# Optimization experiments

Hardware: AMD Instinct MI355X
Metric: run time of the kernel (lower is better)

## Reference

```python
import jax, jax.numpy as jnp
import numpy as np
from jax import lax

B, S, DIMS, T, K = 4, 4096, 2048, 10, 2


def setup_inputs() -> dict:
    key = jax.random.key(0)
    ks = jax.random.split(key, 4)
    scale = 1.0 / np.sqrt(DIMS)
    x = jax.random.normal(ks[0], (B, S, DIMS), dtype=jnp.float32)
    W_cls = jax.random.normal(ks[1], (DIMS, T), dtype=jnp.float32) * scale
    W_sparse = jax.random.normal(ks[2], (DIMS, T), dtype=jnp.float32) * scale
    W_gates = jax.random.normal(ks[3], (DIMS, T), dtype=jnp.float32) * scale
    return {
        "x": x,
        "W_cls": W_cls, "b_cls": jnp.zeros((T,), jnp.float32),
        "W_sparse": W_sparse, "b_sparse": jnp.zeros((T,), jnp.float32),
        "W_gates": W_gates, "b_gates": jnp.zeros((T,), jnp.float32),
        "alpha": jnp.ones((1,), jnp.float32),
    }


def reference(x, W_cls, b_cls, W_sparse, b_sparse, W_gates, b_gates, alpha):
    # soft routing: softmax classifier over num_types
    soft_types = jax.nn.softmax(jnp.einsum("bsd,dt->bst", x, W_cls) + b_cls, axis=-1)
    # sparse routing: top-k over logits, softmax over the k kept logits,
    # scattered back into a dense [B,S,T] gate vector (zeros elsewhere)
    logits = jnp.einsum("bsd,dt->bst", x, W_sparse) + b_sparse
    top_v, top_i = lax.top_k(logits, K)                      # [B,S,K]
    sparse_g = jax.nn.softmax(top_v, axis=-1)                # [B,S,K]
    # scatter via one-hot (K and T are tiny)
    sparse_types = jnp.sum(jax.nn.one_hot(top_i, T, dtype=x.dtype) * sparse_g[..., None], axis=-2)  # [B,S,T]
    # per-type sigmoid gates: batched single matmul == stack of Linear(dims,1)+Sigmoid
    gates = jax.nn.sigmoid(jnp.einsum("bsd,dt->bst", x, W_gates) + b_gates)  # [B,S,T]
    a = jax.nn.sigmoid(alpha)                                # [1], broadcasts
    mixed_types = a * sparse_types + (1.0 - a) * soft_types  # [B,S,T]
    # original: gates stacked as [B,S,1,T], mixed unsqueezed to [B,S,1,T], sum over T -> [B,S,1]
    return jnp.sum(gates * mixed_types, axis=-1, keepdims=True)
```

## Files before the change

kernel.cpp:

```cpp
#include <hip/hip_runtime.h>
#include <math.h>


#define NROWS   16384
#define DIMS_   2048
#define TT      10
#define WAVES   4
#define BLOCK   (WAVES * 64)
#define DGRP    8
#define DPW     (DIMS_ / DGRP / WAVES)
#define DC      16
#define NCH     (DPW / DC)
#define PITCH   17

__global__ __launch_bounds__(BLOCK)
void tgate_k1(const float* __restrict__ x,
              const float* __restrict__ W_cls,
              const float* __restrict__ W_sparse,
              const float* __restrict__ W_gates,
              float* __restrict__ ws)
{
    __shared__ float tile[WAVES * 64 * PITCH];

    const int tid  = threadIdx.x;
    const int lane = tid & 63;
    const int wv   = __builtin_amdgcn_readfirstlane(tid >> 6);
    const int row0 = blockIdx.x * 64;
    const int d0   = blockIdx.y * (DIMS_ / DGRP) + wv * DPW;
    float* tile_w  = &tile[wv * 64 * PITCH];

    float acc[30];
    #pragma unroll
    for (int j = 0; j < 30; ++j) acc[j] = 0.0f;

    const float4* x4 = reinterpret_cast<const float4*>(x);
    const int rl = lane >> 2;
    const int c4 = lane & 3;

    float4 pre[4];
    #pragma unroll
    for (int i = 0; i < 4; ++i) {
        int rr = i * 16 + rl;
        pre[i] = x4[(size_t)(row0 + rr) * (DIMS_ / 4) + (d0 >> 2) + c4];
    }

    for (int c = 0; c < NCH; ++c) {
        #pragma unroll
        for (int i = 0; i < 4; ++i) {
            int rr = i * 16 + rl;
            float* dst = tile_w + rr * PITCH + c4 * 4;
            dst[0] = pre[i].x; dst[1] = pre[i].y; dst[2] = pre[i].z; dst[3] = pre[i].w;
        }
        if (c + 1 < NCH) {
            #pragma unroll
            for (int i = 0; i < 4; ++i) {
                int rr = i * 16 + rl;
                pre[i] = x4[(size_t)(row0 + rr) * (DIMS_ / 4) + ((d0 + (c + 1) * DC) >> 2) + c4];
            }
        }
        const int dg = d0 + c * DC;
        #pragma unroll
        for (int dd = 0; dd < DC; ++dd) {
            float xv = tile_w[lane * PITCH + dd];
            const float* wc = W_cls    + (size_t)(dg + dd) * TT;
            const float* wsp= W_sparse + (size_t)(dg + dd) * TT;
            const float* wg = W_gates  + (size_t)(dg + dd) * TT;
            #pragma unroll
            for (int t = 0; t < TT; ++t) acc[t]      = fmaf(xv, wc[t],  acc[t]);
            #pragma unroll
            for (int t = 0; t < TT; ++t) acc[10 + t] = fmaf(xv, wsp[t], acc[10 + t]);
            #pragma unroll
            for (int t = 0; t < TT; ++t) acc[20 + t] = fmaf(xv, wg[t],  acc[20 + t]);
        }
    }

    float* part = tile;
    __syncthreads();
    if (wv >= 2) {
        float* p = part + (size_t)((wv - 2) * 64 + lane) * 31;
        #pragma unroll
        for (int j = 0; j < 30; ++j) p[j] = acc[j];
    }
    __syncthreads();
    if (wv < 2) {
        const float* p = part + (size_t)(wv * 64 + lane) * 31;
        #pragma unroll
        for (int j = 0; j < 30; ++j) acc[j] += p[j];
    }
    __syncthreads();
    if (wv == 1) {
        float* p = part + (size_t)lane * 31;
        #pragma unroll
        for (int j = 0; j < 30; ++j) p[j] = acc[j];
    }
    __syncthreads();
    if (wv == 0) {
        const float* p = part + (size_t)lane * 31;
        #pragma unroll
        for (int j = 0; j < 30; ++j) acc[j] += p[j];
        float4* w4 = reinterpret_cast<float4*>(ws);
        size_t base = ((size_t)blockIdx.y * NROWS + row0 + lane) * 8;
        #pragma unroll
        for (int q = 0; q < 8; ++q) {
            float a0 = (q * 4 + 0 < 30) ? acc[q * 4 + 0] : 0.0f;
            float a1 = (q * 4 + 1 < 30) ? acc[q * 4 + 1] : 0.0f;
            float a2 = (q * 4 + 2 < 30) ? acc[q * 4 + 2] : 0.0f;
            float a3 = (q * 4 + 3 < 30) ? acc[q * 4 + 3] : 0.0f;
            w4[base + q] = make_float4(a0, a1, a2, a3);
        }
    }
}

__global__ __launch_bounds__(256)
void tgate_k2(const float* __restrict__ ws,
              const float* __restrict__ b_cls,
              const float* __restrict__ b_sparse,
              const float* __restrict__ b_gates,
              const float* __restrict__ alpha,
              float* __restrict__ out)
{
    const int r = blockIdx.x * 256 + threadIdx.x;
    const float4* w4 = reinterpret_cast<const float4*>(ws);

    float l[32];
    #pragma unroll
    for (int j = 0; j < 32; ++j) l[j] = 0.0f;
    #pragma unroll
    for (int s = 0; s < DGRP; ++s) {
        size_t base = ((size_t)s * NROWS + r) * 8;
        #pragma unroll
        for (int q = 0; q < 8; ++q) {
            float4 v = w4[base + q];
            l[q * 4 + 0] += v.x; l[q * 4 + 1] += v.y;
            l[q * 4 + 2] += v.z; l[q * 4 + 3] += v.w;
        }
    }

    float lc[TT], lsp[TT], g[TT];
    #pragma unroll
    for (int t = 0; t < TT; ++t) {
        lc[t]  = l[t]      + b_cls[t];
        lsp[t] = l[10 + t] + b_sparse[t];
        float lg = l[20 + t] + b_gates[t];
        g[t] = 1.0f / (1.0f + __expf(-lg));
    }
    float m = lc[0];
    #pragma unroll
    for (int t = 1; t < TT; ++t) m = fmaxf(m, lc[t]);
    float esum = 0.0f, gdot = 0.0f;
    #pragma unroll
    for (int t = 0; t < TT; ++t) {
        float e = __expf(lc[t] - m);
        esum += e;
        gdot = fmaf(g[t], e, gdot);
    }
    float v1 = lsp[0], v2 = -1e30f, gv1 = g[0], gv2 = 0.0f;
    #pragma unroll
    for (int t = 1; t < TT; ++t) {
        if (lsp[t] > v1)      { v2 = v1; gv2 = gv1; v1 = lsp[t]; gv1 = g[t]; }
        else if (lsp[t] > v2) { v2 = lsp[t]; gv2 = g[t]; }
    }
    float s1 = 1.0f / (1.0f + __expf(v2 - v1));
    float s2 = 1.0f - s1;
    float a  = 1.0f / (1.0f + __expf(-alpha[0]));
    float sparse_dot = fmaf(gv1, s1, gv2 * s2);
    out[r] = fmaf(a, sparse_dot, (1.0f - a) * (gdot / esum));
}

extern "C" void kernel_launch(void* const* d_in, const int* in_sizes, int n_in,
                              void* d_out, int out_size, void* d_ws, size_t ws_size,
                              hipStream_t stream) {
    const float* x        = (const float*)d_in[0];
    const float* W_cls    = (const float*)d_in[1];
    const float* b_cls    = (const float*)d_in[2];
    const float* W_sparse = (const float*)d_in[3];
    const float* b_sparse = (const float*)d_in[4];
    const float* W_gates  = (const float*)d_in[5];
    const float* b_gates  = (const float*)d_in[6];
    const float* alpha    = (const float*)d_in[7];
    float* out = (float*)d_out;
    float* ws  = (float*)d_ws;

    dim3 g1(NROWS / 64, DGRP);
    tgate_k1<<<g1, dim3(BLOCK), 0, stream>>>(x, W_cls, W_sparse, W_gates, ws);

    dim3 g2(NROWS / 256);
    tgate_k2<<<g2, dim3(256), 0, stream>>>(ws, b_cls, b_sparse, b_gates, alpha, out);
}
```

Measured before the change: 250.8 us.

## Stage weights in LDS and register-tile four rows per lane

Each block now covers 256 rows instead of 64. It stages its slice of all three weight matrices into shared memory, packed at 32 floats per dim so they can be read as float4. Each lane accumulates four rows, so every weight read is reused across four rows instead of being reloaded per row from global or scalar memory. The x tile is stored transposed so the per-dim reads are conflict-free. The cross-wave reduction and the workspace layout (now SoA by q-slot) are rewritten to match. The change uses 120 accumulator registers per lane, which risks lower occupancy or spills, and the grid shrinks to 512 blocks.

```diff
diff --git a/kernel.cpp b/kernel.cpp
--- a/kernel.cpp
+++ b/kernel.cpp
@@ -8,10 +8,12 @@
 #define WAVES   4
 #define BLOCK   (WAVES * 64)
 #define DGRP    8
-#define DPW     (DIMS_ / DGRP / WAVES)
-#define DC      16
+#define DBLK    (DIMS_ / DGRP)
+#define DPW     (DBLK / WAVES)
+#define DC      8
 #define NCH     (DPW / DC)
-#define PITCH   17
+#define RPB     256
+#define RPL     4
 
 __global__ __launch_bounds__(BLOCK)
 void tgate_k1(const float* __restrict__ x,
@@ -20,94 +22,133 @@
               const float* __restrict__ W_gates,
               float* __restrict__ ws)
 {
-    __shared__ float tile[WAVES * 64 * PITCH];
+    __shared__ float xt[WAVES][DC][RPB];
+    __shared__ float Wl[DBLK * 32];
 
     const int tid  = threadIdx.x;
     const int lane = tid & 63;
     const int wv   = __builtin_amdgcn_readfirstlane(tid >> 6);
-    const int row0 = blockIdx.x * 64;
-    const int d0   = blockIdx.y * (DIMS_ / DGRP) + wv * DPW;
-    float* tile_w  = &tile[wv * 64 * PITCH];
-
-    float acc[30];
-    #pragma unroll
-    for (int j = 0; j < 30; ++j) acc[j] = 0.0f;
+    const int row0 = blockIdx.x * RPB;
+    const int gy   = blockIdx.y;
+    const int d0w  = gy * DBLK + wv * DPW;
+
+    {
+        const float* Wm[3] = { W_cls, W_sparse, W_gates };
+        #pragma unroll
+        for (int m = 0; m < 3; ++m) {
+            const float* src = Wm[m] + (size_t)gy * DBLK * TT;
+            #pragma unroll
+            for (int it = 0; it < DBLK * TT / BLOCK; ++it) {
+                int f = it * BLOCK + tid;
+                int d = f / TT, t = f - d * TT;
+                Wl[d * 32 + m * TT + t] = src[f];
+            }
+        }
+    }
+
+    float acc[RPL][TT * 3];
+    #pragma unroll
+    for (int r = 0; r < RPL; ++r)
+        #pragma unroll
+        for (int j = 0; j < 30; ++j) acc[r][j] = 0.0f;
 
     const float4* x4 = reinterpret_cast<const float4*>(x);
-    const int rl = lane >> 2;
-    const int c4 = lane & 3;
-
-    float4 pre[4];
-    #pragma unroll
-    for (int i = 0; i < 4; ++i) {
-        int rr = i * 16 + rl;
-        pre[i] = x4[(size_t)(row0 + rr) * (DIMS_ / 4) + (d0 >> 2) + c4];
-    }
+    const int rhalf = lane >> 1;
+    const int dpart = (lane & 1) * 4;
+
+    float4 pre[8];
+    #pragma unroll
+    for (int i = 0; i < 8; ++i)
+        pre[i] = x4[(size_t)(row0 + i * 32 + rhalf) * (DIMS_ / 4) + ((d0w + dpart) >> 2)];
+
+    __syncthreads();
 
     for (int c = 0; c < NCH; ++c) {
         #pragma unroll
-        for (int i = 0; i < 4; ++i) {
-            int rr = i * 16 + rl;
-            float* dst = tile_w + rr * PITCH + c4 * 4;
-            dst[0] = pre[i].x; dst[1] = pre[i].y; dst[2] = pre[i].z; dst[3] = pre[i].w;
+        for (int i = 0; i < 8; ++i) {
+            int rl = i * 32 + rhalf;
+            xt[wv][dpart + 0][rl] = pre[i].x;
+            xt[wv][dpart + 1][rl] = pre[i].y;
+            xt[wv][dpart + 2][rl] = pre[i].z;
+            xt[wv][dpart + 3][rl] = pre[i].w;
         }
         if (c + 1 < NCH) {
             #pragma unroll
-            for (int i = 0; i < 4; ++i) {
-                int rr = i * 16 + rl;
-                pre[i] = x4[(size_t)(row0 + rr) * (DIMS_ / 4) + ((d0 + (c + 1) * DC) >> 2) + c4];
+            for (int i = 0; i < 8; ++i)
+                pre[i] = x4[(size_t)(row0 + i * 32 + rhalf) * (DIMS_ / 4)
+                            + ((d0w + (c + 1) * DC + dpart) >> 2)];
+        }
+        const int dl0 = wv * DPW + c * DC;
+        #pragma unroll
+        for (int dd = 0; dd < DC; ++dd) {
+            float xv[RPL];
+            #pragma unroll
+            for (int r = 0; r < RPL; ++r) xv[r] = xt[wv][dd][lane + 64 * r];
+            const float4* wr = reinterpret_cast<const float4*>(&Wl[(dl0 + dd) * 32]);
+            #pragma unroll
+            for (int q = 0; q < 8; ++q) {
+                float4 w = wr[q];
+                #pragma unroll
+                for (int r = 0; r < RPL; ++r) {
+                    if (q * 4 + 0 < 30) acc[r][q * 4 + 0] = fmaf(xv[r], w.x, acc[r][q * 4 + 0]);
+                    if (q * 4 + 1 < 30) acc[r][q * 4 + 1] = fmaf(xv[r], w.y, acc[r][q * 4 + 1]);
+                    if (q * 4 + 2 < 30) acc[r][q * 4 + 2] = fmaf(xv[r], w.z, acc[r][q * 4 + 2]);
+                    if (q * 4 + 3 < 30) acc[r][q * 4 + 3] = fmaf(xv[r], w.w, acc[r][q * 4 + 3]);
+                }
             }
         }
-        const int dg = d0 + c * DC;
-        #pragma unroll
-        for (int dd = 0; dd < DC; ++dd) {
-            float xv = tile_w[lane * PITCH + dd];
-            const float* wc = W_cls    + (size_t)(dg + dd) * TT;
-            const float* wsp= W_sparse + (size_t)(dg + dd) * TT;
-            const float* wg = W_gates  + (size_t)(dg + dd) * TT;
-            #pragma unroll
-            for (int t = 0; t < TT; ++t) acc[t]      = fmaf(xv, wc[t],  acc[t]);
-            #pragma unroll
-            for (int t = 0; t < TT; ++t) acc[10 + t] = fmaf(xv, wsp[t], acc[10 + t]);
-            #pragma unroll
-            for (int t = 0; t < TT; ++t) acc[20 + t] = fmaf(xv, wg[t],  acc[20 + t]);
-        }
-    }
-
-    float* part = tile;
+    }
+
+    float* red = &xt[0][0][0];
     __syncthreads();
-    if (wv >= 2) {
-        float* p = part + (size_t)((wv - 2) * 64 + lane) * 31;
-        #pragma unroll
-        for (int j = 0; j < 30; ++j) p[j] = acc[j];
-    }
-    __syncthreads();
-    if (wv < 2) {
-        const float* p = part + (size_t)(wv * 64 + lane) * 31;
-        #pragma unroll
-        for (int j = 0; j < 30; ++j) acc[j] += p[j];
-    }
-    __syncthreads();
-    if (wv == 1) {
-        float* p = part + (size_t)lane * 31;
-        #pragma unroll
-        for (int j = 0; j < 30; ++j) p[j] = acc[j];
-    }
-    __syncthreads();
+    for (int p = 0; p < 4; ++p) {
+        if (wv > 0) {
+            int widx = (wv - 1) * 64 + lane;
+            #pragma unroll
+            for (int qq = 0; qq < 2; ++qq)
+                #pragma unroll
+                for (int r = 0; r < RPL; ++r)
+                    #pragma unroll
+                    for (int cm = 0; cm < 4; ++cm) {
+                        int t = (2 * p + qq) * 4 + cm;
+                        float v = (t < 30) ? acc[r][t] : 0.0f;
+                        red[((qq * 4 + r) * 4 + cm) * 192 + widx] = v;
+                    }
+        }
+        __syncthreads();
+        if (wv == 0) {
+            #pragma unroll
+            for (int qq = 0; qq < 2; ++qq)
+                #pragma unroll
+                for (int r = 0; r < RPL; ++r)
+                    #pragma unroll
+                    for (int cm = 0; cm < 4; ++cm) {
+                        int t = (2 * p + qq) * 4 + cm;
+                        if (t < 30) {
+                            float s = acc[r][t];
+                            #pragma unroll
+                            for (int w = 1; w < WAVES; ++w)
+                                s += red[((qq * 4 + r) * 4 + cm) * 192 + (w - 1) * 64 + lane];
+                            acc[r][t] = s;
+                        }
+                    }
+        }
+        __syncthreads();
+    }
+
     if (wv == 0) {
-        const float* p = part + (size_t)lane * 31;
-        #pragma unroll
-        for (int j = 0; j < 30; ++j) acc[j] += p[j];
-        float4* w4 = reinterpret_cast<float4*>(ws);
-        size_t base = ((size_t)blockIdx.y * NROWS + row0 + lane) * 8;
-        #pragma unroll
-        for (int q = 0; q < 8; ++q) {
-            float a0 = (q * 4 + 0 < 30) ? acc[q * 4 + 0] : 0.0f;
-            float a1 = (q * 4 + 1 < 30) ? acc[q * 4 + 1] : 0.0f;
-            float a2 = (q * 4 + 2 < 30) ? acc[q * 4 + 2] : 0.0f;
-            float a3 = (q * 4 + 3 < 30) ? acc[q * 4 + 3] : 0.0f;
-            w4[base + q] = make_float4(a0, a1, a2, a3);
-        }
+        float4* ws4 = reinterpret_cast<float4*>(ws);
+        #pragma unroll
+        for (int q = 0; q < 8; ++q)
+            #pragma unroll
+            for (int r = 0; r < RPL; ++r) {
+                float a0 = acc[r][q * 4 + 0];
+                float a1 = acc[r][q * 4 + 1];
+                float a2 = (q * 4 + 2 < 30) ? acc[r][q * 4 + 2] : 0.0f;
+                float a3 = (q * 4 + 3 < 30) ? acc[r][q * 4 + 3] : 0.0f;
+                ws4[(size_t)(gy * 8 + q) * NROWS + row0 + 64 * r + lane] =
+                    make_float4(a0, a1, a2, a3);
+            }
     }
 }
 
@@ -126,15 +167,13 @@
     #pragma unroll
     for (int j = 0; j < 32; ++j) l[j] = 0.0f;
     #pragma unroll
-    for (int s = 0; s < DGRP; ++s) {
-        size_t base = ((size_t)s * NROWS + r) * 8;
+    for (int gy = 0; gy < DGRP; ++gy)
         #pragma unroll
         for (int q = 0; q < 8; ++q) {
-            float4 v = w4[base + q];
+            float4 v = w4[(size_t)(gy * 8 + q) * NROWS + r];
             l[q * 4 + 0] += v.x; l[q * 4 + 1] += v.y;
             l[q * 4 + 2] += v.z; l[q * 4 + 3] += v.w;
         }
-    }
 
     float lc[TT], lsp[TT], g[TT];
     #pragma unroll
@@ -181,7 +220,7 @@
     float* out = (float*)d_out;
     float* ws  = (float*)d_ws;
 
-    dim3 g1(NROWS / 64, DGRP);
+    dim3 g1(NROWS / RPB, DGRP);
     tgate_k1<<<g1, dim3(BLOCK), 0, stream>>>(x, W_cls, W_sparse, W_gates, ws);
 
     dim3 g2(NROWS / 256);
```

After: 240.9 us. 1.04x faster.
